# Kernel tuning notes

Measured on AMD Instinct MI355X. Metric: run time of the kernel, lower is better.

The kernel has to match this reference:

```python
import jax, jax.numpy as jnp
import numpy as np
from jax.scipy.linalg import solve_triangular

OMEGA0 = 30.0  # standard SIREN first-layer frequency


def setup_inputs() -> dict:
    key = jax.random.key(0)
    ks = jax.random.split(key, 12)
    B, NC, NT, XD, H, R = 64, 1024, 1024, 1, 512, 512
    x_context = jax.random.normal(ks[0], (B, NC, XD), jnp.float32)
    y_context = jax.random.normal(ks[1], (B, NC, 1), jnp.float32)
    x_target = jax.random.normal(ks[2], (B, NT, XD), jnp.float32)
    # SIREN MLP params (hidden_dims=[512,512,512], repr_dim=512)
    def lin(k, fi, fo, first=False):
        bound = 1.0 / fi if first else np.sqrt(6.0 / fi) / OMEGA0
        kW, kb = jax.random.split(k)
        W = jax.random.uniform(kW, (fi, fo), jnp.float32, -bound, bound)
        b = jax.random.uniform(kb, (fo,), jnp.float32, -bound, bound)
        return W, b
    W0, b0 = lin(ks[3], XD, H, first=True)
    W1, b1 = lin(ks[4], H, H)
    W2, b2 = lin(ks[5], H, H)
    Wr, br = lin(ks[6], H, R)
    log_noise_var = jnp.asarray(np.log(0.01), jnp.float32)
    return {"x_context": x_context, "y_context": y_context, "x_target": x_target,
            "W0": W0, "b0": b0, "W1": W1, "b1": b1, "W2": W2, "b2": b2,
            "Wr": Wr, "br": br, "log_noise_var": log_noise_var}


def _mlp(x, W0, b0, W1, b1, W2, b2, Wr, br):
    # SIREN: sine activations, omega_0 on first layer, linear head
    h = jnp.sin(OMEGA0 * (x @ W0 + b0))
    h = jnp.sin(h @ W1 + b1)
    h = jnp.sin(h @ W2 + b2)
    return h @ Wr + br


def reference(x_context, y_context, x_target, W0, b0, W1, b1, W2, b2, Wr, br, log_noise_var):
    mean = jnp.mean(y_context, axis=1, keepdims=True)          # [B,1,1]
    std = jnp.std(y_context, axis=1, keepdims=True, ddof=1)    # torch.std is unbiased
    yc = (y_context - mean) / std                              # [B,N,1]

    cr = _mlp(x_context, W0, b0, W1, b1, W2, b2, Wr, br)       # [B,N,R]
    tr = _mlp(x_target, W0, b0, W1, b1, W2, b2, Wr, br)        # [B,M,R]
    ones_c = jnp.ones(cr.shape[:-1] + (1,), cr.dtype)
    ones_t = jnp.ones(tr.shape[:-1] + (1,), tr.dtype)
    cr = jnp.concatenate([cr, ones_c], axis=-1)                # [B,N,R+1]
    tr = jnp.concatenate([tr, ones_t], axis=-1)                # [B,M,R+1]

    Rp1 = cr.shape[-1]
    cov = jnp.einsum('bnr,bns->brs', cr, cr)                   # [B,R+1,R+1]
    cov = cov + jnp.exp(log_noise_var) * jnp.eye(Rp1, dtype=cov.dtype)
    xty = jnp.einsum('bnr,bnd->brd', cr, yc)                   # [B,R+1,1]

    chol = jnp.linalg.cholesky(cov)                            # batched potrf
    z = solve_triangular(chol, xty, lower=True)
    w = solve_triangular(jnp.swapaxes(chol, -1, -2), z, lower=False)  # [B,R+1,1]

    y_pred = tr @ w                                            # [B,M,1]
    return y_pred * std + mean
```

## Files before the change

kernel.cpp:

```cpp
#include <hip/hip_runtime.h>
#include <hip/hip_fp16.h>
#include <math.h>

#define NB    64
#define NPTS  1024
#define HD    512
#define CPAD  576
#define COVE  ((size_t)NB*CPAD*CPAD)

typedef __attribute__((ext_vector_type(4))) float v4f;
typedef __attribute__((ext_vector_type(8))) short v8s;
typedef __attribute__((ext_vector_type(8))) _Float16 v8h;

__device__ __forceinline__ float sin_poly(float z){
  float t = z*z;
  float p = fmaf(t, -1.9841270e-4f, 8.3333333e-3f);
  p = fmaf(t, p, -0.16666667f);
  p = fmaf(t, p, 1.0f);
  return z*p;
}

__device__ __forceinline__ ushort2 split_f16(float a){
  _Float16 h = (_Float16)a;
  float hf = (float)h;
  _Float16 l = (_Float16)(a - hf);
  unsigned short uh, ul;
  __builtin_memcpy(&uh, &h, 2);
  __builtin_memcpy(&ul, &l, 2);
  ushort2 r; r.x = uh; r.y = ul;
  return r;
}

__device__ __forceinline__ unsigned short f16b(float a){
  _Float16 h = (_Float16)a;
  unsigned short uh; __builtin_memcpy(&uh, &h, 2);
  return uh;
}

__device__ __forceinline__ float f16r(float a){
  return (float)(_Float16)a;
}

__device__ __forceinline__ void g2l16(const unsigned short* g, unsigned short* l){
  __builtin_amdgcn_global_load_lds(
      (const __attribute__((address_space(1))) unsigned int*)(g),
      (__attribute__((address_space(3))) unsigned int*)(l), 16, 0, 0);
}

__global__ __launch_bounds__(256)
void prep_k(const float* __restrict__ W1, const float* __restrict__ W2,
            const float* __restrict__ Wr, unsigned short* __restrict__ wf,
            const float* __restrict__ y, float* __restrict__ meanv,
            float* __restrict__ stdv, float* __restrict__ ycb)
{
  __shared__ unsigned short tile[64][65];
  __shared__ float rs[4], rss[4], bc[2];
  const int tid = threadIdx.x;
  if (blockIdx.x >= 192){
    const int b = blockIdx.x - 192;
    const float* yb = y + (size_t)b*NPTS;
    float4 v = *(const float4*)(yb + tid*4);
    float s  = v.x+v.y+v.z+v.w;
    float ss = v.x*v.x+v.y*v.y+v.z*v.z+v.w*v.w;
    #pragma unroll
    for (int off=32; off; off>>=1){ s += __shfl_down(s, off); ss += __shfl_down(ss, off); }
    int wid = tid>>6, lane = tid&63;
    if (lane == 0){ rs[wid]=s; rss[wid]=ss; }
    __syncthreads();
    if (tid == 0){
      float S  = rs[0]+rs[1]+rs[2]+rs[3];
      float SS = rss[0]+rss[1]+rss[2]+rss[3];
      float mean = S * (1.0f/NPTS);
      float var  = (SS - S*S*(1.0f/NPTS)) * (1.0f/(NPTS-1));
      float sd = sqrtf(var);
      meanv[b]=mean; stdv[b]=sd; bc[0]=mean; bc[1]=1.0f/sd;
    }
    __syncthreads();
    float mean=bc[0], inv=bc[1];
    float4 o;
    o.x=(v.x-mean)*inv; o.y=(v.y-mean)*inv; o.z=(v.z-mean)*inv; o.w=(v.w-mean)*inv;
    *(float4*)(ycb + (size_t)b*NPTS + tid*4) = o;
    return;
  }
  const int mat = blockIdx.x >> 6;
  const int t = blockIdx.x & 63;
  const int k0 = (t >> 3)*64, n0 = (t & 7)*64;
  const float* W = (mat==0) ? W1 : ((mat==1) ? W2 : Wr);
  for (int idx=tid; idx<4096; idx+=256){
    int r = idx >> 6, c = idx & 63;
    tile[r][c] = f16b(W[(size_t)(k0+r)*512 + n0 + c]);
  }
  __syncthreads();
  unsigned short* dst = wf + (size_t)mat*262144;
  for (int idx=tid; idx<4096; idx+=256){
    int r = idx >> 6, c = idx & 63;
    dst[(size_t)(n0+r)*512 + k0 + c] = tile[c][r];
  }
}

__device__ __forceinline__ void h0c(const float* __restrict__ w0,
                                    const float* __restrict__ b0, int K0, int sq,
                                    float xv0, float xv1, v8s& pa0, v8s& pa1)
{
  const float* wp = w0 + K0 + sq*8;
  const float* bp = b0 + K0 + sq*8;
  float4 wva = *(const float4*)wp, wvb = *(const float4*)(wp+4);
  float4 bva = *(const float4*)bp, bvb = *(const float4*)(bp+4);
  float w8[8] = {wva.x,wva.y,wva.z,wva.w,wvb.x,wvb.y,wvb.z,wvb.w};
  float b8[8] = {bva.x,bva.y,bva.z,bva.w,bvb.x,bvb.y,bvb.z,bvb.w};
  #pragma unroll
  for (int i=0;i<8;++i){
    pa0[i] = (short)f16b(__sinf(30.f*fmaf(xv0, w8[i], b8[i])));
    pa1[i] = (short)f16b(__sinf(30.f*fmaf(xv1, w8[i], b8[i])));
  }
}

template<int EPI, int TRANS, int AMODE>
__global__ __launch_bounds__(256, 2)
void gemm_ld(const unsigned short* __restrict__ Ap,
             const float* __restrict__ xsrc, const float* __restrict__ w0,
             const float* __restrict__ b0,
             const unsigned short* __restrict__ Bw,
             const float* __restrict__ bias,
             unsigned short* __restrict__ Chi, unsigned short* __restrict__ Clo,
             const float* __restrict__ vvp, float* __restrict__ ydot, int rowBase)
{
  __shared__ unsigned short Ah[2][4096], Bh[2][8192];
  const int tid  = threadIdx.x;
  const int lane = tid & 63, wave = tid >> 6;
  const int wm = wave & 1, wn = wave >> 1;
  const int m0 = blockIdx.x*128, n0 = blockIdx.y*256;
  const int q = lane >> 4, ln16 = lane & 15;
  const int sr = tid >> 2, sq = tid & 3;
  const int qx  = (q ^ ((ln16>>1)&3))*8;
  const int swc = ((lane&3) ^ ((lane>>3)&3))*8;
  const int wsl = (sq ^ ((sr>>1)&3))*8;

  const int strowA = wave*32 + (lane>>2);
  const int strowB = wave*64 + (lane>>2);
  const unsigned short* gA = Ap + (size_t)(m0 + strowA)*512 + swc;
  const unsigned short* gB = Bw + (size_t)(n0 + strowB)*512 + swc;

  float xv0 = 0.f, xv1 = 0.f;
  if (AMODE == 1){ xv0 = xsrc[m0 + sr]; xv1 = xsrc[m0 + sr + 64]; }

  v4f acc[4][8];
  #pragma unroll
  for (int a=0;a<4;++a)
    #pragma unroll
    for (int b=0;b<8;++b) acc[a][b] = (v4f)(0.0f);

  v8s pa0, pa1;
  if (AMODE == 0){
    g2l16(gA, Ah[0]+wave*1024); g2l16(gA+16*512, Ah[0]+wave*1024+512);
  } else {
    h0c(w0, b0, 0, sq, xv0, xv1, pa0, pa1);
    *(v8s*)(Ah[0] + sr*32 + wsl) = pa0;
    *(v8s*)(Ah[0] + (sr+64)*32 + wsl) = pa1;
  }
  #pragma unroll
  for (int m=0;m<4;++m) g2l16(gB + m*16*512, Bh[0]+wave*2048 + m*512);
  __syncthreads();

  int cur = 0;
  for (int ks=0; ks<16; ++ks){
    const int nxt = cur^1;
    if (ks < 15){
      const int k1 = (ks+1)*32;
      if (AMODE == 0){
        g2l16(gA+k1, Ah[nxt]+wave*1024); g2l16(gA+k1+16*512, Ah[nxt]+wave*1024+512);
      }
      #pragma unroll
      for (int m=0;m<4;++m) g2l16(gB + k1 + m*16*512, Bh[nxt]+wave*2048 + m*512);
    }
    v8h bhf[8];
    #pragma unroll
    for (int nt=0; nt<8; ++nt){
      const int nrow = wn*128 + nt*16 + ln16;
      bhf[nt] = *(const v8h*)(Bh[cur] + nrow*32 + qx);
    }
    #pragma unroll
    for (int mt=0; mt<4; ++mt){
      const int mrow = wm*64 + mt*16 + ln16;
      v8h ah = *(const v8h*)(Ah[cur] + mrow*32 + qx);
      #pragma unroll
      for (int nt=0; nt<8; ++nt)
        acc[mt][nt] = __builtin_amdgcn_mfma_f32_16x16x32_f16(ah, bhf[nt], acc[mt][nt], 0,0,0);
    }
    if (AMODE == 1 && ks < 15){
      h0c(w0, b0, (ks+1)*32, sq, xv0, xv1, pa0, pa1);
      *(v8s*)(Ah[nxt] + sr*32 + wsl) = pa0;
      *(v8s*)(Ah[nxt] + (sr+64)*32 + wsl) = pa1;
    }
    __syncthreads();
    cur = nxt;
  }

  if (TRANS == 0){
    #pragma unroll
    for (int nt=0;nt<8;++nt){
      const int col = n0 + wn*128 + nt*16 + ln16;
      const float bl_ = bias[col];
      #pragma unroll
      for (int mt=0;mt<4;++mt){
        const int row0 = m0 + wm*64 + mt*16 + q*4;
        #pragma unroll
        for (int r=0;r<4;++r){
          float v = acc[mt][nt][r] + bl_;
          if (EPI == 1) v = sin_poly(v);
          Chi[(size_t)(row0+r)*512 + col] = f16b(v);
        }
      }
    }
  } else if (TRANS == 1){
    const int lb = m0 >> 10;
    #pragma unroll
    for (int nt=0;nt<8;++nt){
      const int col = n0 + wn*128 + nt*16 + ln16;
      const float bl_ = bias[col];
      #pragma unroll
      for (int mt=0;mt<4;++mt){
        const int row0 = m0 + wm*64 + mt*16 + q*4;
        const int nb = row0 & 1023;
        ushort4 h,l; ushort2 s;
        s=split_f16(acc[mt][nt][0]+bl_); h.x=s.x; l.x=s.y;
        s=split_f16(acc[mt][nt][1]+bl_); h.y=s.x; l.y=s.y;
        s=split_f16(acc[mt][nt][2]+bl_); h.z=s.x; l.z=s.y;
        s=split_f16(acc[mt][nt][3]+bl_); h.w=s.x; l.w=s.y;
        size_t o = ((size_t)lb*512 + col)*1024 + nb;
        *(ushort4*)(Chi + o) = h;
        *(ushort4*)(Clo + o) = l;
      }
    }
  } else {
    const int b = (rowBase + m0) >> 10;
    const float* vb = vvp + (size_t)b*512;
    float vcol[8];
    float bl_[8];
    #pragma unroll
    for (int nt=0;nt<8;++nt){
      const int col = n0 + wn*128 + nt*16 + ln16;
      vcol[nt] = vb[col];
      bl_[nt] = bias[col];
    }
    #pragma unroll
    for (int mt=0;mt<4;++mt){
      #pragma unroll
      for (int r=0;r<4;++r){
        float part = 0.f;
        #pragma unroll
        for (int nt=0;nt<8;++nt)
          part = fmaf(sin_poly(acc[mt][nt][r] + bl_[nt]), vcol[nt], part);
        #pragma unroll
        for (int off=1; off<16; off<<=1) part += __shfl_xor(part, off, 64);
        if (ln16 == 0){
          const int row = m0 + wm*64 + mt*16 + q*4 + r;
          atomicAdd(&ydot[rowBase + row], part);
        }
      }
    }
  }
}

__device__ __forceinline__ void ld_ext_row(const unsigned short* __restrict__ h,
                                           const unsigned short* __restrict__ l,
                                           const float* __restrict__ ycn,
                                           int f, int nofs, v8s& oh, v8s& ol)
{
  if (f < 512){
    oh = *(const v8s*)(h + (size_t)f*1024 + nofs);
    ol = *(const v8s*)(l + (size_t)f*1024 + nofs);
  } else if (f == 512){
    #pragma unroll
    for (int j=0;j<8;++j){ oh[j] = (short)0x3C00; ol[j] = 0; }
  } else if (f == 513){
    #pragma unroll
    for (int j=0;j<8;++j){
      ushort2 s = split_f16(ycn[nofs+j]);
      oh[j] = (short)s.x; ol[j] = (short)s.y;
    }
  } else {
    #pragma unroll
    for (int j=0;j<8;++j){ oh[j] = 0; ol[j] = 0; }
  }
}

__global__ __launch_bounds__(256)
void cov_ld(const unsigned short* __restrict__ CThi, const unsigned short* __restrict__ CTlo,
            const float* __restrict__ ycb,
            const float* __restrict__ lnv, float* __restrict__ cov, int bStart)
{
  int t = blockIdx.y;
  int ti = 0;
  while ((ti+1)*(ti+2)/2 <= t) ++ti;
  int tj = t - ti*(ti+1)/2;
  const int i0 = ti*128, j0 = tj*128;
  const int lb = blockIdx.x;
  const int b  = bStart + lb;
  const unsigned short* srch = CThi + (size_t)lb*512*1024;
  const unsigned short* srcl = CTlo + (size_t)lb*512*1024;
  const float* ycn = ycb + (size_t)b*NPTS;
  float* covb = cov + (size_t)b*CPAD*CPAD;
  const float noise = expf(lnv[0]);
  const bool diag = (i0 == j0);
  const bool aReg = (i0 == 512);

  __shared__ unsigned short Ah[2][4096], Al[2][4096], Bh2[2][4096], Bl2[2][4096];
  const int tid = threadIdx.x;
  const int lane = tid & 63, wave = tid >> 6;
  const int wm = wave & 1, wn = wave >> 1;
  const int q = lane >> 4, ln16 = lane & 15;
  const int sr = tid >> 2, sq = tid & 3;
  const int qx  = (q ^ ((ln16>>1)&3))*8;
  const int swc = ((lane&3) ^ ((lane>>3)&3))*8;
  const int wsl = (sq ^ ((sr>>1)&3))*8;
  const bool skipW = diag && (wave == 2);

  const int strow = wave*32 + (lane>>2);
  const size_t gaOff = (size_t)(i0 + strow)*1024 + swc;
  const size_t gbOff = (size_t)(j0 + strow)*1024 + swc;
  const int wb = wave*1024;

  v4f acc[4][4];
  #pragma unroll
  for (int a=0;a<4;++a)
    #pragma unroll
    for (int c=0;c<4;++c) acc[a][c] = (v4f)(0.0f);

  if (!aReg){
    g2l16(srch + gaOff, Ah[0]+wb); g2l16(srch + gaOff + (size_t)16*1024, Ah[0]+wb+512);
    g2l16(srcl + gaOff, Al[0]+wb); g2l16(srcl + gaOff + (size_t)16*1024, Al[0]+wb+512);
  } else {
    v8s th, tl;
    ld_ext_row(srch, srcl, ycn, i0 + sr, sq*8, th, tl);
    *(v8s*)(Ah[0] + sr*32 + wsl) = th; *(v8s*)(Al[0] + sr*32 + wsl) = tl;
    ld_ext_row(srch, srcl, ycn, i0 + sr + 64, sq*8, th, tl);
    *(v8s*)(Ah[0] + (sr+64)*32 + wsl) = th; *(v8s*)(Al[0] + (sr+64)*32 + wsl) = tl;
  }
  if (!diag){
    g2l16(srch + gbOff, Bh2[0]+wb); g2l16(srch + gbOff + (size_t)16*1024, Bh2[0]+wb+512);
    g2l16(srcl + gbOff, Bl2[0]+wb); g2l16(srcl + gbOff + (size_t)16*1024, Bl2[0]+wb+512);
  }
  __syncthreads();

  int cur = 0;
  for (int ks=0; ks<32; ++ks){
    const int nxt = cur^1;
    if (ks < 31){
      const int k1 = (ks+1)*32;
      if (!aReg){
        g2l16(srch + gaOff + k1, Ah[nxt]+wb);
        g2l16(srch + gaOff + k1 + (size_t)16*1024, Ah[nxt]+wb+512);
        g2l16(srcl + gaOff + k1, Al[nxt]+wb);
        g2l16(srcl + gaOff + k1 + (size_t)16*1024, Al[nxt]+wb+512);
      }
      if (!diag){
        g2l16(srch + gbOff + k1, Bh2[nxt]+wb);
        g2l16(srch + gbOff + k1 + (size_t)16*1024, Bh2[nxt]+wb+512);
        g2l16(srcl + gbOff + k1, Bl2[nxt]+wb);
        g2l16(srcl + gbOff + k1 + (size_t)16*1024, Bl2[nxt]+wb+512);
      }
    }
    if (!skipW){
      const unsigned short* BhP = diag ? Ah[cur] : Bh2[cur];
      const unsigned short* BlP = diag ? Al[cur] : Bl2[cur];
      v8h bhf[4], blf[4];
      #pragma unroll
      for (int nt=0; nt<4; ++nt){
        const int nrow = wn*64 + nt*16 + ln16;
        bhf[nt] = *(const v8h*)(BhP + nrow*32 + qx);
        blf[nt] = *(const v8h*)(BlP + nrow*32 + qx);
      }
      #pragma unroll
      for (int mt=0; mt<4; ++mt){
        const int mrow = wm*64 + mt*16 + ln16;
        v8h ah = *(const v8h*)(Ah[cur] + mrow*32 + qx);
        v8h al = *(const v8h*)(Al[cur] + mrow*32 + qx);
        #pragma unroll
        for (int nt=0; nt<4; ++nt){
          acc[mt][nt] = __builtin_amdgcn_mfma_f32_16x16x32_f16(ah, bhf[nt], acc[mt][nt], 0,0,0);
          acc[mt][nt] = __builtin_amdgcn_mfma_f32_16x16x32_f16(ah, blf[nt], acc[mt][nt], 0,0,0);
          acc[mt][nt] = __builtin_amdgcn_mfma_f32_16x16x32_f16(al, bhf[nt], acc[mt][nt], 0,0,0);
        }
      }
    }
    if (aReg && ks < 31){
      const int n1 = (ks+1)*32 + sq*8;
      v8s th, tl;
      ld_ext_row(srch, srcl, ycn, i0 + sr, n1, th, tl);
      *(v8s*)(Ah[nxt] + sr*32 + wsl) = th; *(v8s*)(Al[nxt] + sr*32 + wsl) = tl;
      ld_ext_row(srch, srcl, ycn, i0 + sr + 64, n1, th, tl);
      *(v8s*)(Ah[nxt] + (sr+64)*32 + wsl) = th; *(v8s*)(Al[nxt] + (sr+64)*32 + wsl) = tl;
    }
    __syncthreads();
    cur = nxt;
  }
  #pragma unroll
  for (int nt=0;nt<4;++nt){
    const int gj = j0 + wn*64 + nt*16 + ln16;
    #pragma unroll
    for (int mt=0;mt<4;++mt){
      const int gi0 = i0 + wm*64 + mt*16 + q*4;
      #pragma unroll
      for (int r=0;r<4;++r){
        const int gi = gi0 + r;
        if (gj <= gi && gi < CPAD && gj < CPAD){
          float v = acc[mt][nt][r];
          if (gi == gj) v += (gi < 513) ? noise : 1.0f;
          covb[(size_t)gi*CPAD + gj] = v;
        }
      }
    }
  }
}

__global__ __launch_bounds__(256)
void chol_trsm_k(float* __restrict__ cov, float* __restrict__ dchol, int k)
{
  (void)dchol;
  float* Ab = cov + (size_t)blockIdx.x * CPAD * CPAD;
  const int o = k*64;
  const int row0 = o + 64 + blockIdx.y*128;
  const int nrows = min(128, CPAD - row0);
  __shared__ float Ds[64][65];
  __shared__ float As[128][65];
  __shared__ float invd[64];
  const int tid = threadIdx.x;

  for (int idx=tid; idx<nrows*16; idx+=256){
    int r = idx >> 4, c = (idx & 15)*4;
    float4 v = *(const float4*)(Ab + (size_t)(row0+r)*CPAD + o + c);
    As[r][c]=v.x; As[r][c+1]=v.y; As[r][c+2]=v.z; As[r][c+3]=v.w;
  }

  if (tid < 64){
    float a[64];
    const float* rowp = Ab + (size_t)(o+tid)*CPAD + o;
    #pragma unroll
    for (int c=0; c<64; c+=4){
      float4 v = *(const float4*)(rowp + c);
      a[c]   = (c   <= tid) ? v.x : 0.f;
      a[c+1] = (c+1 <= tid) ? v.y : 0.f;
      a[c+2] = (c+2 <= tid) ? v.z : 0.f;
      a[c+3] = (c+3 <= tid) ? v.w : 0.f;
    }
    #pragma unroll
    for (int j=0; j<63; ++j){
      float vj = a[j];
      float t = vj * (1.0f / __shfl(vj, j, 64));
      #pragma unroll
      for (int c=j+1; c<64; ++c)
        a[c] = fmaf(-t, __shfl(vj, c, 64), a[c]);
    }
    float myinv = 0.f;
    #pragma unroll
    for (int c=0; c<64; ++c){
      float ic = 1.0f / sqrtf(__shfl(a[c], c, 64));
      a[c] *= ic;
      myinv = (c == tid) ? ic : myinv;
    }
    invd[tid] = myinv;
    #pragma unroll
    for (int c=0; c<64; ++c) Ds[tid][c] = a[c];
  }
  __syncthreads();

  const int srow = tid - 64;
  if (srow >= 0 && srow < nrows){
    float x[64];
    #pragma unroll
    for (int c=0; c<64; ++c){
      float s0 = As[srow][c], s1 = 0.f, s2 = 0.f, s3 = 0.f;
      #pragma unroll
      for (int j=0; j+4<=c; j+=4){
        s0 = fmaf(-x[j],   Ds[c][j],   s0);
        s1 = fmaf(-x[j+1], Ds[c][j+1], s1);
        s2 = fmaf(-x[j+2], Ds[c][j+2], s2);
        s3 = fmaf(-x[j+3], Ds[c][j+3], s3);
      }
      #pragma unroll
      for (int j = c & ~3; j < c; ++j)
        s0 = fmaf(-x[j], Ds[c][j], s0);
      x[c] = ((s0+s1)+(s2+s3)) * invd[c];
    }
    #pragma unroll
    for (int c=0; c<64; ++c) As[srow][c] = x[c];
  } else if (blockIdx.y == 0 && tid >= 192){
    const int r = tid - 192;
    float y[64];
    #pragma unroll
    for (int c = 63; c >= 0; --c){
      float s0 = (c == r) ? 1.0f : 0.0f, s1 = 0.f, s2 = 0.f, s3 = 0.f;
      #pragma unroll
      for (int j = c+1; j+4 <= 64; j += 4){
        s0 = fmaf(-Ds[j][c],   y[j],   s0);
        s1 = fmaf(-Ds[j+1][c], y[j+1], s1);
        s2 = fmaf(-Ds[j+2][c], y[j+2], s2);
        s3 = fmaf(-Ds[j+3][c], y[j+3], s3);
      }
      #pragma unroll
      for (int j = c+1 + ((63-c) & ~3); j < 64; ++j)
        s0 = fmaf(-Ds[j][c], y[j], s0);
      y[c] = ((s0+s1)+(s2+s3)) * invd[c];
    }
    float* dst = Ab + (size_t)(o + r)*CPAD + 512;
    #pragma unroll
    for (int c = 0; c < 64; c += 4)
      *(float4*)(dst + c) = make_float4(y[c], y[c+1], y[c+2], y[c+3]);
  }
  __syncthreads();
  for (int idx=tid; idx<nrows*16; idx+=256){
    int r = idx >> 4, c = (idx & 15)*4;
    float4 v = make_float4(As[r][c], As[r][c+1], As[r][c+2], As[r][c+3]);
    *(float4*)(Ab + (size_t)(row0+r)*CPAD + o + c) = v;
  }
}

__global__ __launch_bounds__(256)
void chol_trsmM_k(float* __restrict__ cov, int k)
{
  float* Ab = cov + (size_t)blockIdx.x * CPAD * CPAD;
  const int o = k*64;
  const int row0 = o + 64 + blockIdx.y*128;
  const int nrows = min(128, CPAD - row0);
  __shared__ unsigned short Mh[64*72], Ml[64*72], Ph[128*72], Pl[128*72];
  const int tid = threadIdx.x;
  const int lane = tid & 63, wave = tid >> 6;
  const int q = lane >> 4, ln16 = lane & 15;

  for (int idx=tid; idx<1024; idx+=256){
    int r = idx >> 4, c = (idx & 15)*4;
    float4 v = *(const float4*)(Ab + (size_t)(o+r)*CPAD + 512 + c);
    ushort4 hh, ll; ushort2 s;
    s=split_f16(v.x); hh.x=s.x; ll.x=s.y;
    s=split_f16(v.y); hh.y=s.x; ll.y=s.y;
    s=split_f16(v.z); hh.z=s.x; ll.z=s.y;
    s=split_f16(v.w); hh.w=s.x; ll.w=s.y;
    *(ushort4*)(Mh + r*72 + c) = hh;
    *(ushort4*)(Ml + r*72 + c) = ll;
  }
  for (int idx=tid; idx<nrows*16; idx+=256){
    int r = idx >> 4, c = (idx & 15)*4;
    float4 v = *(const float4*)(Ab + (size_t)(row0+r)*CPAD + o + c);
    ushort4 hh, ll; ushort2 s;
    s=split_f16(v.x); hh.x=s.x; ll.x=s.y;
    s=split_f16(v.y); hh.y=s.x; ll.y=s.y;
    s=split_f16(v.z); hh.z=s.x; ll.z=s.y;
    s=split_f16(v.w); hh.w=s.x; ll.w=s.y;
    *(ushort4*)(Ph + r*72 + c) = hh;
    *(ushort4*)(Pl + r*72 + c) = ll;
  }
  __syncthreads();

  v4f acc[2][4];
  #pragma unroll
  for (int rt=0;rt<2;++rt)
    #pragma unroll
    for (int nt=0;nt<4;++nt) acc[rt][nt] = (v4f)(0.0f);

  #pragma unroll
  for (int ks=0; ks<2; ++ks){
    const int ko = ks*32 + q*8;
    #pragma unroll
    for (int rt=0; rt<2; ++rt){
      const int ar = wave*32 + rt*16 + ln16;
      v8h ah = *(const v8h*)(Ph + ar*72 + ko);
      v8h al = *(const v8h*)(Pl + ar*72 + ko);
      #pragma unroll
      for (int nt=0; nt<4; ++nt){
        v8h bh = *(const v8h*)(Mh + (nt*16 + ln16)*72 + ko);
        v8h bl = *(const v8h*)(Ml + (nt*16 + ln16)*72 + ko);
        acc[rt][nt] = __builtin_amdgcn_mfma_f32_16x16x32_f16(ah, bh, acc[rt][nt], 0,0,0);
        acc[rt][nt] = __builtin_amdgcn_mfma_f32_16x16x32_f16(ah, bl, acc[rt][nt], 0,0,0);
        acc[rt][nt] = __builtin_amdgcn_mfma_f32_16x16x32_f16(al, bh, acc[rt][nt], 0,0,0);
      }
    }
  }

  #pragma unroll
  for (int rt=0; rt<2; ++rt){
    #pragma unroll
    for (int nt=0; nt<4; ++nt){
      #pragma unroll
      for (int r=0; r<4; ++r){
        const int lr = wave*32 + rt*16 + q*4 + r;
        if (lr < nrows)
          Ab[(size_t)(row0+lr)*CPAD + o + nt*16 + ln16] = acc[rt][nt][r];
      }
    }
  }
}

__global__ __launch_bounds__(256)
void chol_trail_k(float* __restrict__ cov, int k)
{
  float* Ab = cov + (size_t)blockIdx.y * CPAD * CPAD;
  int t = blockIdx.x;
  int bi = 0;
  while ((bi+1)*(bi+2)/2 <= t) ++bi;
  int bj = t - bi*(bi+1)/2;
  const int o = k*64;
  const int s0 = o + 64;
  const int I = s0 + bi*64, J = s0 + bj*64;
  const bool diag = (bi == bj);
  const bool term = (bi == 0) && (bj == 0);

  __shared__ unsigned short Pih[64*72], Pil[64*72];
  __shared__ __align__(16) unsigned short PjBuf[2][64*72];
  __shared__ float invl[64];
  unsigned short* Pjh = PjBuf[0];
  unsigned short* Pjl = PjBuf[1];
  float* Ds = (float*)PjBuf;
  const int tid = threadIdx.x;
  const int lane = tid & 63, wave = tid >> 6;
  const int q = lane >> 4, ln16 = lane & 15;

  for (int idx=tid; idx<1024; idx+=256){
    int r = idx >> 4, c = (idx & 15)*4;
    float4 v = *(const float4*)(Ab + (size_t)(I+r)*CPAD + o + c);
    ushort4 hh, ll; ushort2 s;
    s=split_f16(v.x); hh.x=s.x; ll.x=s.y;
    s=split_f16(v.y); hh.y=s.x; ll.y=s.y;
    s=split_f16(v.z); hh.z=s.x; ll.z=s.y;
    s=split_f16(v.w); hh.w=s.x; ll.w=s.y;
    *(ushort4*)(Pih + r*72 + c) = hh;
    *(ushort4*)(Pil + r*72 + c) = ll;
    if (!diag){
      float4 u = *(const float4*)(Ab + (size_t)(J+r)*CPAD + o + c);
      s=split_f16(u.x); hh.x=s.x; ll.x=s.y;
      s=split_f16(u.y); hh.y=s.x; ll.y=s.y;
      s=split_f16(u.z); hh.z=s.x; ll.z=s.y;
      s=split_f16(u.w); hh.w=s.x; ll.w=s.y;
      *(ushort4*)(Pjh + r*72 + c) = hh;
      *(ushort4*)(Pjl + r*72 + c) = ll;
    }
  }
  __syncthreads();
  const unsigned short* Bh = diag ? Pih : Pjh;
  const unsigned short* Bl = diag ? Pil : Pjl;

  v4f acc[4];
  #pragma unroll
  for (int nt=0;nt<4;++nt) acc[nt] = (v4f)(0.0f);

  #pragma unroll
  for (int ks=0; ks<2; ++ks){
    const int ko = ks*32 + q*8;
    v8h ah = *(const v8h*)(Pih + (wave*16 + ln16)*72 + ko);
    v8h al = *(const v8h*)(Pil + (wave*16 + ln16)*72 + ko);
    #pragma unroll
    for (int nt=0; nt<4; ++nt){
      v8h bh = *(const v8h*)(Bh + (nt*16 + ln16)*72 + ko);
      v8h bl = *(const v8h*)(Bl + (nt*16 + ln16)*72 + ko);
      acc[nt] = __builtin_amdgcn_mfma_f32_16x16x32_f16(ah, bh, acc[nt], 0,0,0);
      acc[nt] = __builtin_amdgcn_mfma_f32_16x16x32_f16(ah, bl, acc[nt], 0,0,0);
      acc[nt] = __builtin_amdgcn_mfma_f32_16x16x32_f16(al, bh, acc[nt], 0,0,0);
    }
  }

  if (!term){
    #pragma unroll
    for (int nt=0; nt<4; ++nt){
      const int gj = J + nt*16 + ln16;
      #pragma unroll
      for (int r=0; r<4; ++r){
        const int gi = I + wave*16 + q*4 + r;
        if (gj <= gi)
          Ab[(size_t)gi*CPAD + gj] -= acc[nt][r];
      }
    }
  } else {
    __syncthreads();
    #pragma unroll
    for (int nt=0; nt<4; ++nt){
      const int lj = nt*16 + ln16;
      #pragma unroll
      for (int r=0; r<4; ++r){
        const int li = wave*16 + q*4 + r;
        float u = (lj <= li) ? (Ab[(size_t)(I+li)*CPAD + J+lj] - acc[nt][r]) : 0.f;
        Ds[li*66 + lj] = u;
      }
    }
    __syncthreads();
    if (tid < 64){
      float a[64];
      #pragma unroll
      for (int c=0;c<64;++c) a[c] = Ds[tid*66 + c];
      #pragma unroll
      for (int j=0;j<63;++j){
        float vj = a[j];
        float tt = vj * (1.0f/__shfl(vj, j, 64));
        #pragma unroll
        for (int c=j+1;c<64;++c)
          a[c] = fmaf(-tt, __shfl(vj, c, 64), a[c]);
      }
      float myinv = 0.f;
      #pragma unroll
      for (int c=0;c<64;++c){
        float ic = 1.0f/sqrtf(__shfl(a[c], c, 64));
        a[c] *= ic;
        myinv = (c==tid) ? ic : myinv;
      }
      invl[tid] = myinv;
      #pragma unroll
      for (int c=0;c<64;++c) Ds[tid*66 + c] = a[c];
    }
    __syncthreads();
    if (tid < 64){
      const int r = tid;
      float y[64];
      #pragma unroll
      for (int c=63;c>=0;--c){
        float s0 = (c==r)?1.f:0.f, s1=0.f, s2=0.f, s3=0.f;
        #pragma unroll
        for (int j=c+1;j+4<=64;j+=4){
          s0 = fmaf(-Ds[j*66+c],     y[j],   s0);
          s1 = fmaf(-Ds[(j+1)*66+c], y[j+1], s1);
          s2 = fmaf(-Ds[(j+2)*66+c], y[j+2], s2);
          s3 = fmaf(-Ds[(j+3)*66+c], y[j+3], s3);
        }
        #pragma unroll
        for (int j=c+1+((63-c)&~3); j<64; ++j)
          s0 = fmaf(-Ds[j*66+c], y[j], s0);
        y[c] = ((s0+s1)+(s2+s3)) * invl[c];
      }
      float* dst = Ab + (size_t)(I + r)*CPAD + 512;
      #pragma unroll
      for (int c=0;c<64;c+=4)
        *(float4*)(dst + c) = make_float4(y[c], y[c+1], y[c+2], y[c+3]);
    }
  }
}

__global__ __launch_bounds__(256)
void chol_last_k(float* __restrict__ cov, float* __restrict__ dchol)
{
  float* Ab = cov + (size_t)blockIdx.x * CPAD * CPAD;
  __shared__ float P[64][65];
  __shared__ float Ds[64][65];
  __shared__ float invl[64];
  const int tid = threadIdx.x;

  for (int idx=tid; idx<1024; idx+=256){
    int r = idx >> 4, c = (idx & 15)*4;
    float4 v = *(const float4*)(Ab + (size_t)(512+r)*CPAD + 448 + c);
    P[r][c]=v.x; P[r][c+1]=v.y; P[r][c+2]=v.z; P[r][c+3]=v.w;
    float4 u = *(const float4*)(Ab + (size_t)(512+r)*CPAD + 512 + c);
    Ds[r][c]   = (c   <= r) ? u.x : 0.f;
    Ds[r][c+1] = (c+1 <= r) ? u.y : 0.f;
    Ds[r][c+2] = (c+2 <= r) ? u.z : 0.f;
    Ds[r][c+3] = (c+3 <= r) ? u.w : 0.f;
  }
  __syncthreads();
  {
    const int tx = tid & 15, ty = tid >> 4;
    float acc[4][4];
    #pragma unroll
    for (int r=0;r<4;++r)
      #pragma unroll
      for (int c=0;c<4;++c) acc[r][c]=0.f;
    for (int kk=0; kk<64; ++kk){
      float av[4], bv[4];
      #pragma unroll
      for (int r=0;r<4;++r) av[r] = P[tx*4+r][kk];
      #pragma unroll
      for (int c=0;c<4;++c) bv[c] = P[ty*4+c][kk];
      #pragma unroll
      for (int r=0;r<4;++r)
        #pragma unroll
        for (int c=0;c<4;++c) acc[r][c] = fmaf(av[r], bv[c], acc[r][c]);
    }
    __syncthreads();
    #pragma unroll
    for (int r=0;r<4;++r){
      int gi = tx*4 + r;
      #pragma unroll
      for (int c=0;c<4;++c){
        int gj = ty*4 + c;
        if (gj <= gi) Ds[gi][gj] -= acc[r][c];
      }
    }
  }
  __syncthreads();

  if (tid < 64){
    float a[64];
    #pragma unroll
    for (int c=0; c<64; ++c) a[c] = Ds[tid][c];
    #pragma unroll
    for (int j=0; j<63; ++j){
      float vj = a[j];
      float t = vj * (1.0f / __shfl(vj, j, 64));
      #pragma unroll
      for (int c=j+1; c<64; ++c)
        a[c] = fmaf(-t, __shfl(vj, c, 64), a[c]);
    }
    float myinv = 0.f;
    #pragma unroll
    for (int c=0; c<64; ++c){
      float ic = 1.0f / sqrtf(__shfl(a[c], c, 64));
      a[c] *= ic;
      myinv = (c == tid) ? ic : myinv;
    }
    invl[tid] = myinv;
    #pragma unroll
    for (int c=0; c<64; ++c) Ds[tid][c] = a[c];
  }
  __syncthreads();

  float* dst = dchol + ((size_t)blockIdx.x*9 + 8)*4096;
  for (int idx=tid; idx<4096; idx+=256)
    dst[idx] = Ds[idx>>6][idx&63];
  if (tid < 64){
    const int r = tid;
    float y[64];
    #pragma unroll
    for (int c = 63; c >= 0; --c){
      float s0 = (c == r) ? 1.0f : 0.0f, s1 = 0.f, s2 = 0.f, s3 = 0.f;
      #pragma unroll
      for (int j = c+1; j+4 <= 64; j += 4){
        s0 = fmaf(-Ds[j][c],   y[j],   s0);
        s1 = fmaf(-Ds[j+1][c], y[j+1], s1);
        s2 = fmaf(-Ds[j+2][c], y[j+2], s2);
        s3 = fmaf(-Ds[j+3][c], y[j+3], s3);
      }
      #pragma unroll
      for (int j = c+1 + ((63-c) & ~3); j < 64; ++j)
        s0 = fmaf(-Ds[j][c], y[j], s0);
      y[c] = ((s0+s1)+(s2+s3)) * invl[c];
    }
    float* dst2 = Ab + (size_t)(512 + r)*CPAD + 512;
    #pragma unroll
    for (int c = 0; c < 64; c += 4)
      *(float4*)(dst2 + c) = make_float4(y[c], y[c+1], y[c+2], y[c+3]);
  }
}

__global__ __launch_bounds__(1024)
void back_solve_k(const float* __restrict__ cov, const float* __restrict__ dchol,
                  const float* __restrict__ Wr, const float* __restrict__ br,
                  float* __restrict__ vv, float* __restrict__ cvec,
                  float* __restrict__ ydot)
{
  const int b = blockIdx.x;
  const float* L = cov + (size_t)b*CPAD*CPAD;
  const float* dc = dchol + (size_t)b*9*4096;
  __shared__ float inv2[64*64];
  __shared__ float rhs[CPAD];
  __shared__ float xv[64];
  __shared__ float red[4*512];
  const int tid = threadIdx.x;
  const int pr = tid >> 4, pc = (tid & 15)*4;
  const float* zrow = L + (size_t)513*CPAD;

  for (int i=tid; i<CPAD; i+=1024)
    rhs[i] = (i < 512) ? zrow[i] : ((i == 512) ? dc[8*4096 + 64] : 0.f);
  {
    float4 v = *(const float4*)(L + (size_t)(512 + pr)*CPAD + 512 + pc);
    *(float4*)(inv2 + pr*64 + pc) = v;
  }
  __syncthreads();

  for (int k=8; k>=1; --k){
    const int o = k*64;
    const int G = o >> 2;
    const int act = G << 2;
    float4 v16[16];
    int rg = 0, cg = 0;
    if (tid < act){
      rg = tid / G; cg = tid % G;
      const float* lp = L + (size_t)(o + rg*16)*CPAD + cg*4;
      #pragma unroll
      for (int rr=0; rr<16; ++rr)
        v16[rr] = *(const float4*)(lp + (size_t)rr*CPAD);
    }
    float4 pf = *(const float4*)(L + (size_t)((k-1)*64 + pr)*CPAD + 512 + pc);
    if (tid < 64){
      float acc = 0.f;
      #pragma unroll
      for (int j=0;j<64;++j) acc = fmaf(inv2[j*64 + tid], rhs[o+j], acc);
      xv[tid] = acc;
      rhs[o+tid] = acc;
    }
    __syncthreads();
    if (tid < act){
      float4 s = {0.f,0.f,0.f,0.f};
      #pragma unroll
      for (int rr=0; rr<16; ++rr){
        float xr = xv[rg*16 + rr];
        s.x = fmaf(v16[rr].x, xr, s.x);
        s.y = fmaf(v16[rr].y, xr, s.y);
        s.z = fmaf(v16[rr].z, xr, s.z);
        s.w = fmaf(v16[rr].w, xr, s.w);
      }
      *(float4*)(red + rg*512 + cg*4) = s;
    }
    __syncthreads();
    if (tid < o)
      rhs[tid] -= (red[tid] + red[512+tid]) + (red[1024+tid] + red[1536+tid]);
    *(float4*)(inv2 + pr*64 + pc) = pf;
    __syncthreads();
  }
  if (tid < 64){
    float acc = 0.f;
    #pragma unroll
    for (int j=0;j<64;++j) acc = fmaf(inv2[j*64 + tid], rhs[j], acc);
    rhs[tid] = acc;
  }
  __syncthreads();

  ydot[(size_t)b*1024 + tid] = 0.f;
  const int j = tid >> 1, h = tid & 1;
  {
    float acc = 0.f;
    const float* row = Wr + (size_t)j*512 + h*256;
    const float* wsp = rhs + h*256;
    for (int r=0; r<256; r+=4){
      float4 w4 = *(const float4*)(row + r);
      acc = fmaf(f16r(w4.x), wsp[r],   acc);
      acc = fmaf(f16r(w4.y), wsp[r+1], acc);
      acc = fmaf(f16r(w4.z), wsp[r+2], acc);
      acc = fmaf(f16r(w4.w), wsp[r+3], acc);
    }
    red[tid] = acc;
  }
  __syncthreads();
  if (h == 0) vv[(size_t)b*512 + j] = red[tid] + red[tid+1];
  __syncthreads();
  red[tid] = (tid < 512) ? br[tid]*rhs[tid] : 0.f;
  __syncthreads();
  for (int s2=512; s2>0; s2>>=1){
    if (tid < s2) red[tid] += red[tid+s2];
    __syncthreads();
  }
  if (tid == 0) cvec[b] = red[0] + rhs[512];
}

__global__ __launch_bounds__(256)
void fin_k(const float* __restrict__ ydot, const float* __restrict__ cvec,
           const float* __restrict__ meanv, const float* __restrict__ stdv,
           float* __restrict__ out)
{
  int i = blockIdx.x*256 + threadIdx.x;
  int b = i >> 10;
  out[i] = fmaf(ydot[i] + cvec[b], stdv[b], meanv[b]);
}

extern "C" void kernel_launch(void* const* d_in, const int* in_sizes, int n_in,
                              void* d_out, int out_size, void* d_ws, size_t ws_size,
                              hipStream_t stream)
{
  (void)in_sizes; (void)n_in; (void)out_size;
  const float* x_ctx = (const float*)d_in[0];
  const float* y_ctx = (const float*)d_in[1];
  const float* x_tgt = (const float*)d_in[2];
  const float* W0 = (const float*)d_in[3];
  const float* b0 = (const float*)d_in[4];
  const float* W1 = (const float*)d_in[5];
  const float* b1 = (const float*)d_in[6];
  const float* W2 = (const float*)d_in[7];
  const float* b2 = (const float*)d_in[8];
  const float* Wr = (const float*)d_in[9];
  const float* br = (const float*)d_in[10];
  const float* lnv = (const float*)d_in[11];
  float* out = (float*)d_out;
  float* ws = (float*)d_ws;

  int CH = 65536;
  for (;;){
    size_t fl = COVE + 65536 + 192 + (size_t)64*512 + (size_t)64*CPAD + 65536
              + (size_t)64*9*4096 + 64;
    size_t sh = (size_t)3*262144 + (size_t)2*CH*512 + (size_t)2*(CH/1024)*512*1024;
    size_t need = fl*4 + sh*2;
    if (ws_size >= need || CH <= 1024) break;
    CH >>= 1;
  }
  const int nch = 65536 / CH;
  const int bpc = CH / NPTS;

  float* cov   = ws;
  float* ycb   = cov + COVE;
  float* meanv = ycb + 65536;
  float* stdv  = meanv + 64;
  float* cvec  = stdv + 64;
  float* vvb   = cvec + 64;
  float* wvb   = vvb + (size_t)64*512;
  float* ydot  = wvb + (size_t)64*CPAD;
  float* dchol = ydot + 65536;
  unsigned short* wf   = (unsigned short*)(dchol + (size_t)64*9*4096);
  unsigned short* P0   = wf + (size_t)3*262144;
  unsigned short* P1   = P0 + (size_t)CH*512;
  unsigned short* CThi = P1 + (size_t)CH*512;
  unsigned short* CTlo = CThi + (size_t)bpc*512*1024;

  prep_k<<<256, 256, 0, stream>>>(W1, W2, Wr, wf, y_ctx, meanv, stdv, ycb);

  for (int c=0; c<nch; ++c){
    const float* xc = x_ctx + (size_t)c*CH;
    dim3 g(CH/128, 2);
    gemm_ld<1,0,1><<<g, 256, 0, stream>>>(0, xc, W0, b0, wf, b1, P1, 0, 0, 0, 0);
    gemm_ld<1,0,0><<<g, 256, 0, stream>>>(P1, 0, 0, 0, wf+262144, b2, P0, 0, 0, 0, 0);
    gemm_ld<0,1,0><<<g, 256, 0, stream>>>(P0, 0, 0, 0, wf+524288, br, CThi, CTlo, 0, 0, 0);
    cov_ld<<<dim3(bpc, 15), 256, 0, stream>>>(CThi, CTlo, ycb, lnv, cov, c*bpc);
  }

  {
    chol_trsm_k<<<dim3(NB, 4), 256, 0, stream>>>(cov, dchol, 0);
    chol_trail_k<<<dim3(36, NB), 256, 0, stream>>>(cov, 0);
    for (int k=1; k<7; ++k){
      const int cnt = CPAD - k*64 - 64;
      chol_trsmM_k<<<dim3(NB, (cnt + 127)/128), 256, 0, stream>>>(cov, k);
      const int tcnt = cnt >> 6;
      chol_trail_k<<<dim3(tcnt*(tcnt+1)/2, NB), 256, 0, stream>>>(cov, k);
    }
    chol_trsmM_k<<<dim3(NB, 1), 256, 0, stream>>>(cov, 7);
  }
  chol_last_k<<<NB, 256, 0, stream>>>(cov, dchol);
  back_solve_k<<<NB, 1024, 0, stream>>>(cov, dchol, Wr, br, vvb, cvec, ydot);

  for (int c=0; c<nch; ++c){
    const float* xt = x_tgt + (size_t)c*CH;
    dim3 g(CH/128, 2);
    gemm_ld<1,0,1><<<g, 256, 0, stream>>>(0, xt, W0, b0, wf, b1, P1, 0, 0, 0, 0);
    gemm_ld<1,2,0><<<g, 256, 0, stream>>>(P1, 0, 0, 0, wf+262144, b2, 0, 0, vvb, ydot, c*CH);
  }
  fin_k<<<256, 256, 0, stream>>>(ydot, cvec, meanv, stdv, out);
}
```

Baseline: 1.248 ms.

## Split diagonal-block Cholesky factorization out of trailing-update kernel

Removes the fused 'term' path from chol_trail_k, where one trailing block also factorized and inverted the next 64x64 diagonal block. That work moves into a dedicated 64-thread chol_fact_k launched after each trailing update, and the host loop is reorganized to run trail, then fact, then panel TRSM per step. The aim is to shrink register and LDS demand in the trailing-update kernel so all its blocks run at higher occupancy, and to remove the long-running outlier block that sets that kernel's tail. The cost is seven extra small kernel launches on the serial critical path of the factorization.

After: 1.083 ms. 1.15x faster.

```diff
diff --git a/kernel.cpp b/kernel.cpp
--- a/kernel.cpp
+++ b/kernel.cpp
@@ -516,6 +516,68 @@
   }
 }
 
+__global__ __launch_bounds__(64)
+void chol_fact_k(float* __restrict__ cov, int k)
+{
+  float* Ab = cov + (size_t)blockIdx.x * CPAD * CPAD;
+  const int o = k*64;
+  __shared__ float Ds[64][65];
+  __shared__ float invd[64];
+  const int tid = threadIdx.x;
+
+  float a[64];
+  const float* rowp = Ab + (size_t)(o+tid)*CPAD + o;
+  #pragma unroll
+  for (int c=0; c<64; c+=4){
+    float4 v = *(const float4*)(rowp + c);
+    a[c]   = (c   <= tid) ? v.x : 0.f;
+    a[c+1] = (c+1 <= tid) ? v.y : 0.f;
+    a[c+2] = (c+2 <= tid) ? v.z : 0.f;
+    a[c+3] = (c+3 <= tid) ? v.w : 0.f;
+  }
+  #pragma unroll
+  for (int j=0; j<63; ++j){
+    float vj = a[j];
+    float t = vj * (1.0f / __shfl(vj, j, 64));
+    #pragma unroll
+    for (int c=j+1; c<64; ++c)
+      a[c] = fmaf(-t, __shfl(vj, c, 64), a[c]);
+  }
+  float myinv = 0.f;
+  #pragma unroll
+  for (int c=0; c<64; ++c){
+    float ic = 1.0f / sqrtf(__shfl(a[c], c, 64));
+    a[c] *= ic;
+    myinv = (c == tid) ? ic : myinv;
+  }
+  invd[tid] = myinv;
+  #pragma unroll
+  for (int c=0; c<64; ++c) Ds[tid][c] = a[c];
+  __syncthreads();
+
+  const int r = tid;
+  float y[64];
+  #pragma unroll
+  for (int c = 63; c >= 0; --c){
+    float s0 = (c == r) ? 1.0f : 0.0f, s1 = 0.f, s2 = 0.f, s3 = 0.f;
+    #pragma unroll
+    for (int j = c+1; j+4 <= 64; j += 4){
+      s0 = fmaf(-Ds[j][c],   y[j],   s0);
+      s1 = fmaf(-Ds[j+1][c], y[j+1], s1);
+      s2 = fmaf(-Ds[j+2][c], y[j+2], s2);
+      s3 = fmaf(-Ds[j+3][c], y[j+3], s3);
+    }
+    #pragma unroll
+    for (int j = c+1 + ((63-c) & ~3); j < 64; ++j)
+      s0 = fmaf(-Ds[j][c], y[j], s0);
+    y[c] = ((s0+s1)+(s2+s3)) * invd[c];
+  }
+  float* dst = Ab + (size_t)(o + r)*CPAD + 512;
+  #pragma unroll
+  for (int c = 0; c < 64; c += 4)
+    *(float4*)(dst + c) = make_float4(y[c], y[c+1], y[c+2], y[c+3]);
+}
+
 __global__ __launch_bounds__(256)
 void chol_trsmM_k(float* __restrict__ cov, int k)
 {
@@ -603,14 +665,8 @@
   const int s0 = o + 64;
   const int I = s0 + bi*64, J = s0 + bj*64;
   const bool diag = (bi == bj);
-  const bool term = (bi == 0) && (bj == 0);
-
-  __shared__ unsigned short Pih[64*72], Pil[64*72];
-  __shared__ __align__(16) unsigned short PjBuf[2][64*72];
-  __shared__ float invl[64];
-  unsigned short* Pjh = PjBuf[0];
-  unsigned short* Pjl = PjBuf[1];
-  float* Ds = (float*)PjBuf;
+
+  __shared__ unsigned short Pih[64*72], Pil[64*72], Pjh[64*72], Pjl[64*72];
   const int tid = threadIdx.x;
   const int lane = tid & 63, wave = tid >> 6;
   const int q = lane >> 4, ln16 = lane & 15;
@@ -658,76 +714,14 @@
     }
   }
 
-  if (!term){
-    #pragma unroll
-    for (int nt=0; nt<4; ++nt){
-      const int gj = J + nt*16 + ln16;
-      #pragma unroll
-      for (int r=0; r<4; ++r){
-        const int gi = I + wave*16 + q*4 + r;
-        if (gj <= gi)
-          Ab[(size_t)gi*CPAD + gj] -= acc[nt][r];
-      }
-    }
-  } else {
-    __syncthreads();
-    #pragma unroll
-    for (int nt=0; nt<4; ++nt){
-      const int lj = nt*16 + ln16;
-      #pragma unroll
-      for (int r=0; r<4; ++r){
-        const int li = wave*16 + q*4 + r;
-        float u = (lj <= li) ? (Ab[(size_t)(I+li)*CPAD + J+lj] - acc[nt][r]) : 0.f;
-        Ds[li*66 + lj] = u;
-      }
-    }
-    __syncthreads();
-    if (tid < 64){
-      float a[64];
-      #pragma unroll
-      for (int c=0;c<64;++c) a[c] = Ds[tid*66 + c];
-      #pragma unroll
-      for (int j=0;j<63;++j){
-        float vj = a[j];
-        float tt = vj * (1.0f/__shfl(vj, j, 64));
-        #pragma unroll
-        for (int c=j+1;c<64;++c)
-          a[c] = fmaf(-tt, __shfl(vj, c, 64), a[c]);
-      }
-      float myinv = 0.f;
-      #pragma unroll
-      for (int c=0;c<64;++c){
-        float ic = 1.0f/sqrtf(__shfl(a[c], c, 64));
-        a[c] *= ic;
-        myinv = (c==tid) ? ic : myinv;
-      }
-      invl[tid] = myinv;
-      #pragma unroll
-      for (int c=0;c<64;++c) Ds[tid*66 + c] = a[c];
-    }
-    __syncthreads();
-    if (tid < 64){
-      const int r = tid;
-      float y[64];
-      #pragma unroll
-      for (int c=63;c>=0;--c){
-        float s0 = (c==r)?1.f:0.f, s1=0.f, s2=0.f, s3=0.f;
-        #pragma unroll
-        for (int j=c+1;j+4<=64;j+=4){
-          s0 = fmaf(-Ds[j*66+c],     y[j],   s0);
-          s1 = fmaf(-Ds[(j+1)*66+c], y[j+1], s1);
-          s2 = fmaf(-Ds[(j+2)*66+c], y[j+2], s2);
-          s3 = fmaf(-Ds[(j+3)*66+c], y[j+3], s3);
-        }
-        #pragma unroll
-        for (int j=c+1+((63-c)&~3); j<64; ++j)
-          s0 = fmaf(-Ds[j*66+c], y[j], s0);
-        y[c] = ((s0+s1)+(s2+s3)) * invl[c];
-      }
-      float* dst = Ab + (size_t)(I + r)*CPAD + 512;
-      #pragma unroll
-      for (int c=0;c<64;c+=4)
-        *(float4*)(dst + c) = make_float4(y[c], y[c+1], y[c+2], y[c+3]);
+  #pragma unroll
+  for (int nt=0; nt<4; ++nt){
+    const int gj = J + nt*16 + ln16;
+    #pragma unroll
+    for (int r=0; r<4; ++r){
+      const int gi = I + wave*16 + q*4 + r;
+      if (gj <= gi)
+        Ab[(size_t)gi*CPAD + gj] -= acc[nt][r];
     }
   }
 }
@@ -1006,14 +1000,13 @@
 
   {
     chol_trsm_k<<<dim3(NB, 4), 256, 0, stream>>>(cov, dchol, 0);
-    chol_trail_k<<<dim3(36, NB), 256, 0, stream>>>(cov, 0);
-    for (int k=1; k<7; ++k){
-      const int cnt = CPAD - k*64 - 64;
-      chol_trsmM_k<<<dim3(NB, (cnt + 127)/128), 256, 0, stream>>>(cov, k);
-      const int tcnt = cnt >> 6;
+    for (int k=0; k<7; ++k){
+      const int tcnt = (CPAD - k*64 - 64) >> 6;
       chol_trail_k<<<dim3(tcnt*(tcnt+1)/2, NB), 256, 0, stream>>>(cov, k);
-    }
-    chol_trsmM_k<<<dim3(NB, 1), 256, 0, stream>>>(cov, 7);
+      chol_fact_k<<<NB, 64, 0, stream>>>(cov, k+1);
+      const int cnt2 = CPAD - (k+1)*64 - 64;
+      chol_trsmM_k<<<dim3(NB, (cnt2 + 127)/128), 256, 0, stream>>>(cov, k+1);
+    }
   }
   chol_last_k<<<NB, 256, 0, stream>>>(cov, dchol);
   back_solve_k<<<NB, 1024, 0, stream>>>(cov, dchol, Wr, br, vvb, cvec, ydot);
```
